# Optimization experiments

Hardware: AMD Instinct MI355X
Metric: run time of the kernel (lower is better)

Reference implementation:

```python
import jax, jax.numpy as jnp
import numpy as np

WIN = 3  # win_size from init


def setup_inputs() -> dict:
    key = jax.random.key(0)
    ks = jax.random.split(key, 7)
    B, H, W, d = 8, 128, 128, 128
    N = H * W
    s = d ** -0.5  # param init scale
    return {
        "x": jax.random.normal(ks[0], (B, N, d), dtype=jnp.float32),
        "Wq": jax.random.normal(ks[1], (d, d), dtype=jnp.float32) * s,
        "bq": jax.random.normal(ks[2], (d,), dtype=jnp.float32) * 0.01,
        "Wk": jax.random.normal(ks[3], (d, d), dtype=jnp.float32) * s,
        "bk": jax.random.normal(ks[4], (d,), dtype=jnp.float32) * 0.01,
        "Wv": jax.random.normal(ks[5], (d, d), dtype=jnp.float32) * s,
        "bv": jax.random.normal(ks[6], (d,), dtype=jnp.float32) * 0.01,
        "H": H,
        "W": W,
    }


def reference(x, Wq, bq, Wk, bk, Wv, bv, H, W):
    B, N, d = x.shape
    scale = d ** -0.5
    pad = WIN // 2

    q = (x @ Wq + bq).reshape(B, H, W, d)
    k = (x @ Wk + bk).reshape(B, H, W, d)
    v = (x @ Wv + bv).reshape(B, H, W, d)

    # zero-pad spatial dims (matches F.pad); padded neighbors get logit 0, not -inf
    k_pad = jnp.pad(k, ((0, 0), (pad, pad), (pad, pad), (0, 0)))
    v_pad = jnp.pad(v, ((0, 0), (pad, pad), (pad, pad), (0, 0)))

    scores_l, vs_l = [], []
    for dy in range(WIN):
        for dx in range(WIN):
            k_slice = k_pad[:, dy:dy + H, dx:dx + W]   # [B,H,W,d]
            v_slice = v_pad[:, dy:dy + H, dx:dx + W]
            scores_l.append(jnp.einsum("bhwd,bhwd->bhw", q, k_slice) * scale)
            vs_l.append(v_slice)

    scores = jnp.stack(scores_l, axis=-1)            # [B,H,W,9]
    prob = jax.nn.softmax(scores, axis=-1)           # [B,H,W,9]
    v_stk = jnp.stack(vs_l, axis=-1)                 # [B,H,W,d,9]
    out = jnp.einsum("bhwn,bhwdn->bhwd", prob, v_stk)
    return out.reshape(B, N, d)
```

## Files before the change

kernel.cpp:

```cpp
#include <hip/hip_runtime.h>
#include <stdint.h>

#define B_ 8
#define H_ 128
#define W_ 128
#define D_ 128
#define N_ (H_*W_)
#define M_ (B_*N_)

typedef __attribute__((ext_vector_type(8))) short short8;
typedef __attribute__((ext_vector_type(4))) float floatx4;

typedef const __attribute__((address_space(1))) void* gas_t;
typedef __attribute__((address_space(3))) void* las_t;

__device__ inline unsigned short f2bf(float f){
  union { float f; unsigned int i; } c; c.f = f;
  unsigned int x = c.i;
  x += 0x7FFF + ((x >> 16) & 1);
  return (unsigned short)(x >> 16);
}
__device__ inline float bflo(unsigned int u){
  union { unsigned int i; float f; } c; c.i = u << 16; return c.f;
}
__device__ inline float bfhi(unsigned int u){
  union { unsigned int i; float f; } c; c.i = u & 0xFFFF0000u; return c.f;
}

__global__ void wtrans_kernel(const float* __restrict__ Wq, const float* __restrict__ Wk,
                              const float* __restrict__ Wv, unsigned short* __restrict__ Wt){
  const float* src = blockIdx.x == 0 ? Wq : (blockIdx.x == 1 ? Wk : Wv);
  unsigned short* dst = Wt + blockIdx.x * (D_*D_);
  const int i = blockIdx.y * 256 + threadIdx.x;
  const int k = i >> 7, n = i & 127;
  dst[n*D_ + k] = f2bf(src[i]);
}

__global__ __launch_bounds__(256, 3) void qkv_gemm_kernel(
    const float* __restrict__ x, const unsigned short* __restrict__ Wt,
    const float* __restrict__ bq, const float* __restrict__ bk, const float* __restrict__ bv,
    unsigned short* __restrict__ Q, unsigned short* __restrict__ K, unsigned short* __restrict__ V)
{
  const int rowTile = blockIdx.x;

  __shared__ unsigned short lds[24576];

  const int t = threadIdx.x;
  const int wave = t >> 6, lane = t & 63;

  {
    const unsigned short* W0 = Wt;
    #pragma unroll
    for (int p = 0; p < 8; ++p){
      int s = p*256 + t;
      int n = s >> 4, cp = s & 15, c = cp ^ (n & 7);
      const unsigned short* gp = W0 + n*128 + c*8;
      unsigned short* lp = (unsigned short*)lds + 8192 + p*2048 + wave*512;
      __builtin_amdgcn_global_load_lds((gas_t)(const void*)gp, (las_t)(void*)lp, 16, 0, 0);
    }
  }

  {
    const float* xrow = x + (size_t)rowTile * 64 * D_;
    #pragma unroll
    for (int p = 0; p < 4; ++p){
      int s = p*256 + t;
      int r = s >> 4, cp = s & 15, c = cp ^ (r & 7);
      const float* gp = xrow + r*D_ + c*8;
      float4 f0 = *(const float4*)gp;
      float4 f1 = *(const float4*)(gp + 4);
      uint4 pk;
      pk.x = (unsigned)f2bf(f0.x) | ((unsigned)f2bf(f0.y) << 16);
      pk.y = (unsigned)f2bf(f0.z) | ((unsigned)f2bf(f0.w) << 16);
      pk.z = (unsigned)f2bf(f1.x) | ((unsigned)f2bf(f1.y) << 16);
      pk.w = (unsigned)f2bf(f1.z) | ((unsigned)f2bf(f1.w) << 16);
      *(uint4*)&lds[s*8] = pk;
    }
  }
  __syncthreads();

  const int wm = (wave >> 1) * 32, wn = (wave & 1) * 64;
  const int m0 = lane & 15, quad = lane >> 4;

  #pragma unroll
  for (int which = 0; which < 3; ++which){
    floatx4 acc[4][2] = {};
    #pragma unroll
    for (int kk = 0; kk < 4; ++kk){
      short8 a[2], b[4];
      #pragma unroll
      for (int i = 0; i < 2; ++i){
        int row = wm + i*16 + m0;
        int c = (kk*4 + quad) ^ (row & 7);
        a[i] = *(const short8*)&lds[row*128 + c*8];
      }
      #pragma unroll
      for (int j = 0; j < 4; ++j){
        int n = wn + j*16 + m0;
        int c = (kk*4 + quad) ^ (n & 7);
        b[j] = *(const short8*)&lds[8192 + n*128 + c*8];
      }
      #pragma unroll
      for (int j = 0; j < 4; ++j)
        #pragma unroll
        for (int i = 0; i < 2; ++i)
          acc[j][i] = __builtin_amdgcn_mfma_f32_16x16x32_bf16(b[j], a[i], acc[j][i], 0, 0, 0);
    }
    __syncthreads();

    if (which < 2){
      const unsigned short* Wnext = Wt + (which + 1) * (D_*D_);
      #pragma unroll
      for (int p = 0; p < 8; ++p){
        int s = p*256 + t;
        int n = s >> 4, cp = s & 15, c = cp ^ (n & 7);
        const unsigned short* gp = Wnext + n*128 + c*8;
        unsigned short* lp = (unsigned short*)lds + 8192 + p*2048 + wave*512;
        __builtin_amdgcn_global_load_lds((gas_t)(const void*)gp, (las_t)(void*)lp, 16, 0, 0);
      }
    }

    {
      const float* bias = which == 0 ? bq : (which == 1 ? bk : bv);
      unsigned short* Out = which == 0 ? Q : (which == 1 ? K : V);
      unsigned short* Outp = Out + (size_t)rowTile * 64 * D_;
      #pragma unroll
      for (int j = 0; j < 4; ++j){
        const float4 bb = *(const float4*)&bias[wn + j*16 + quad*4];
        #pragma unroll
        for (int i = 0; i < 2; ++i){
          const int row = wm + i*16 + m0;
          uint2 pk;
          pk.x = (unsigned)f2bf(acc[j][i][0] + bb.x) | ((unsigned)f2bf(acc[j][i][1] + bb.y) << 16);
          pk.y = (unsigned)f2bf(acc[j][i][2] + bb.z) | ((unsigned)f2bf(acc[j][i][3] + bb.w) << 16);
          *(uint2*)(Outp + row*D_ + wn + j*16 + quad*4) = pk;
        }
      }
    }

    if (which < 2) __syncthreads();
  }
}

__global__ __launch_bounds__(256, 2) void attn_kernel(
    const unsigned short* __restrict__ Q, const unsigned short* __restrict__ K,
    const unsigned short* __restrict__ V, float* __restrict__ out)
{
  const int t = threadIdx.x;
  const int e8 = t & 7;
  const int pix = blockIdx.x * 32 + (t >> 3);
  const int w = pix & 127;
  const int h = (pix >> 7) & 127;
  const int bbase = pix & ~(N_ - 1);
  const float scale = 0.08838834764831845f;
  const int doff = e8 * 16;
  const size_t off = (size_t)pix * D_ + doff;

  int npix[9]; bool okm[9];
  #pragma unroll
  for (int i = 0; i < 9; ++i){
    const int dy = i/3 - 1, dx = i%3 - 1;
    const int hh = h + dy, ww = w + dx;
    okm[i] = ((unsigned)hh < 128u) && ((unsigned)ww < 128u);
    const int hc = min(max(hh, 0), 127);
    const int wc = min(max(ww, 0), 127);
    npix[i] = bbase + hc*W_ + wc;
  }

  uint4 qu0, qu1;
  {
    const unsigned short* qp = Q + off;
    qu0 = *(const uint4*)qp;
    qu1 = *(const uint4*)(qp + 8);
  }
  uint4 ku[9][2];
  #pragma unroll
  for (int i = 0; i < 9; ++i){
    const unsigned short* kp = K + (size_t)npix[i]*D_ + doff;
    ku[i][0] = *(const uint4*)kp;
    ku[i][1] = *(const uint4*)(kp + 8);
  }
  uint4 vu[9][2];
  #pragma unroll
  for (int i = 0; i < 9; ++i){
    const unsigned short* vp = V + (size_t)npix[i]*D_ + doff;
    vu[i][0] = *(const uint4*)vp;
    vu[i][1] = *(const uint4*)(vp + 8);
  }

  float q[16];
  {
    unsigned uu[8] = {qu0.x, qu0.y, qu0.z, qu0.w, qu1.x, qu1.y, qu1.z, qu1.w};
    #pragma unroll
    for (int e = 0; e < 8; ++e){
      q[e*2]     = bflo(uu[e]) * scale;
      q[e*2 + 1] = bfhi(uu[e]) * scale;
    }
  }

  float s[9];
  #pragma unroll
  for (int i = 0; i < 9; ++i){
    unsigned uu[8] = {ku[i][0].x, ku[i][0].y, ku[i][0].z, ku[i][0].w,
                      ku[i][1].x, ku[i][1].y, ku[i][1].z, ku[i][1].w};
    float acc = 0.f;
    #pragma unroll
    for (int e = 0; e < 8; ++e){
      acc += q[e*2]     * bflo(uu[e]);
      acc += q[e*2 + 1] * bfhi(uu[e]);
    }
    s[i] = okm[i] ? acc : 0.f;
  }
  #pragma unroll
  for (int i = 0; i < 9; ++i){
    s[i] += __shfl_xor(s[i], 1, 64);
    s[i] += __shfl_xor(s[i], 2, 64);
    s[i] += __shfl_xor(s[i], 4, 64);
  }

  float m = s[0];
  #pragma unroll
  for (int i = 1; i < 9; ++i) m = fmaxf(m, s[i]);
  float p[9]; float l = 0.f;
  #pragma unroll
  for (int i = 0; i < 9; ++i){ p[i] = __expf(s[i] - m); l += p[i]; }
  const float inv = 1.f / l;

  float o[16];
  #pragma unroll
  for (int d = 0; d < 16; ++d) o[d] = 0.f;
  #pragma unroll
  for (int i = 0; i < 9; ++i){
    const float pi = okm[i] ? p[i] * inv : 0.f;
    unsigned uu[8] = {vu[i][0].x, vu[i][0].y, vu[i][0].z, vu[i][0].w,
                      vu[i][1].x, vu[i][1].y, vu[i][1].z, vu[i][1].w};
    #pragma unroll
    for (int e = 0; e < 8; ++e){
      o[e*2]     += pi * bflo(uu[e]);
      o[e*2 + 1] += pi * bfhi(uu[e]);
    }
  }

  float* op = out + off;
  #pragma unroll
  for (int c = 0; c < 4; ++c){
    float4 v4 = make_float4(o[c*4], o[c*4+1], o[c*4+2], o[c*4+3]);
    *(float4*)(op + c*4) = v4;
  }
}

extern "C" void kernel_launch(void* const* d_in, const int* in_sizes, int n_in,
                              void* d_out, int out_size, void* d_ws, size_t ws_size,
                              hipStream_t stream)
{
  const float* x  = (const float*)d_in[0];
  const float* Wq = (const float*)d_in[1];
  const float* bq = (const float*)d_in[2];
  const float* Wk = (const float*)d_in[3];
  const float* bk = (const float*)d_in[4];
  const float* Wv = (const float*)d_in[5];
  const float* bv = (const float*)d_in[6];
  float* out = (float*)d_out;

  char* ws = (char*)d_ws;
  unsigned short* Wt = (unsigned short*)ws;
  unsigned short* Q  = (unsigned short*)(ws + (1<<17));
  unsigned short* K  = (unsigned short*)(ws + (1<<17) + (size_t)M_*D_*2);
  unsigned short* V  = (unsigned short*)(ws + (1<<17) + (size_t)2*M_*D_*2);

  hipLaunchKernelGGL(wtrans_kernel, dim3(3, 64), dim3(256), 0, stream, Wq, Wk, Wv, Wt);
  hipLaunchKernelGGL(qkv_gemm_kernel, dim3(M_/64), dim3(256), 0, stream,
                     x, Wt, bq, bk, bv, Q, K, V);
  hipLaunchKernelGGL(attn_kernel, dim3(M_/32), dim3(256), 0, stream, Q, K, V, out);
}
```

Before: 201.5 us.

## Load weight fragments directly from global memory instead of staging in LDS

The QKV GEMM no longer stages each 128x128 bf16 weight matrix into shared memory with async global-to-LDS copies. Each wave now reads its B fragments straight from global memory, relying on L2 for reuse. The A fragments of x are hoisted into registers once and reused across Q, K and V, which removes the per-matrix barriers and cuts LDS to 16 KB. In exchange, every block re-reads the full weights from global or L2 memory with uncoalesced 16-byte loads. Register pressure also rises, and launch bounds drop from 3 to 2 blocks per SM.

After: 227.0 us. +12.6%, slower.

```diff
diff --git a/kernel.cpp b/kernel.cpp
--- a/kernel.cpp
+++ b/kernel.cpp
@@ -10,9 +10,6 @@
 
 typedef __attribute__((ext_vector_type(8))) short short8;
 typedef __attribute__((ext_vector_type(4))) float floatx4;
-
-typedef const __attribute__((address_space(1))) void* gas_t;
-typedef __attribute__((address_space(3))) void* las_t;
 
 __device__ inline unsigned short f2bf(float f){
   union { float f; unsigned int i; } c; c.f = f;
@@ -36,29 +33,17 @@
   dst[n*D_ + k] = f2bf(src[i]);
 }
 
-__global__ __launch_bounds__(256, 3) void qkv_gemm_kernel(
+__global__ __launch_bounds__(256, 2) void qkv_gemm_kernel(
     const float* __restrict__ x, const unsigned short* __restrict__ Wt,
     const float* __restrict__ bq, const float* __restrict__ bk, const float* __restrict__ bv,
     unsigned short* __restrict__ Q, unsigned short* __restrict__ K, unsigned short* __restrict__ V)
 {
   const int rowTile = blockIdx.x;
 
-  __shared__ unsigned short lds[24576];
+  __shared__ unsigned short lds[8192];
 
   const int t = threadIdx.x;
   const int wave = t >> 6, lane = t & 63;
-
-  {
-    const unsigned short* W0 = Wt;
-    #pragma unroll
-    for (int p = 0; p < 8; ++p){
-      int s = p*256 + t;
-      int n = s >> 4, cp = s & 15, c = cp ^ (n & 7);
-      const unsigned short* gp = W0 + n*128 + c*8;
-      unsigned short* lp = (unsigned short*)lds + 8192 + p*2048 + wave*512;
-      __builtin_amdgcn_global_load_lds((gas_t)(const void*)gp, (las_t)(void*)lp, 16, 0, 0);
-    }
-  }
 
   {
     const float* xrow = x + (size_t)rowTile * 64 * D_;
@@ -82,42 +67,34 @@
   const int wm = (wave >> 1) * 32, wn = (wave & 1) * 64;
   const int m0 = lane & 15, quad = lane >> 4;
 
+  short8 a[4][2];
+  #pragma unroll
+  for (int kk = 0; kk < 4; ++kk)
+    #pragma unroll
+    for (int i = 0; i < 2; ++i){
+      int row = wm + i*16 + m0;
+      int c = (kk*4 + quad) ^ (row & 7);
+      a[kk][i] = *(const short8*)&lds[row*128 + c*8];
+    }
+
   #pragma unroll
   for (int which = 0; which < 3; ++which){
+    const unsigned short* Wsel = Wt + which * (D_*D_);
+
     floatx4 acc[4][2] = {};
     #pragma unroll
     for (int kk = 0; kk < 4; ++kk){
-      short8 a[2], b[4];
-      #pragma unroll
-      for (int i = 0; i < 2; ++i){
-        int row = wm + i*16 + m0;
-        int c = (kk*4 + quad) ^ (row & 7);
-        a[i] = *(const short8*)&lds[row*128 + c*8];
-      }
+      short8 b[4];
       #pragma unroll
       for (int j = 0; j < 4; ++j){
         int n = wn + j*16 + m0;
-        int c = (kk*4 + quad) ^ (n & 7);
-        b[j] = *(const short8*)&lds[8192 + n*128 + c*8];
+        b[j] = *(const short8*)(Wsel + n*128 + kk*32 + quad*8);
       }
       #pragma unroll
       for (int j = 0; j < 4; ++j)
         #pragma unroll
         for (int i = 0; i < 2; ++i)
-          acc[j][i] = __builtin_amdgcn_mfma_f32_16x16x32_bf16(b[j], a[i], acc[j][i], 0, 0, 0);
-    }
-    __syncthreads();
-
-    if (which < 2){
-      const unsigned short* Wnext = Wt + (which + 1) * (D_*D_);
-      #pragma unroll
-      for (int p = 0; p < 8; ++p){
-        int s = p*256 + t;
-        int n = s >> 4, cp = s & 15, c = cp ^ (n & 7);
-        const unsigned short* gp = Wnext + n*128 + c*8;
-        unsigned short* lp = (unsigned short*)lds + 8192 + p*2048 + wave*512;
-        __builtin_amdgcn_global_load_lds((gas_t)(const void*)gp, (las_t)(void*)lp, 16, 0, 0);
-      }
+          acc[j][i] = __builtin_amdgcn_mfma_f32_16x16x32_bf16(b[j], a[kk][i], acc[j][i], 0, 0, 0);
     }
 
     {
@@ -137,8 +114,6 @@
         }
       }
     }
-
-    if (which < 2) __syncthreads();
   }
 }
 
```
